# Kernel tuning notes

Measured on AMD Instinct MI355X. Metric: run time of the kernel, lower is better.

## Reference

```python
import jax, jax.numpy as jnp
import numpy as np

NEG_SLOPE = 0.01  # F.leaky_relu default
FGW = 0.1         # feature_guidance_weight


def gat_layer(x, src, dst, W, att_l, att_r, heads, out_ch, concat):
    N = x.shape[0]
    # reward-based guidance weights (L1-normalized over nodes, F.normalize p=1 dim=0)
    rw = 1.0 / (jnp.abs(x[:, -1:]) + 1e-6)                    # [N,1]
    rw = rw / jnp.maximum(jnp.sum(jnp.abs(rw), axis=0), 1e-12)
    h = (x @ W).reshape(N, heads, out_ch)                      # [N,H,C]
    # per-node attention halves, gathered per edge (avoids [E,H,C] for scores)
    al = jnp.sum(h * att_l, axis=-1)                           # [N,H] (x_i side)
    ar = jnp.sum(h * att_r, axis=-1)                           # [N,H] (x_j side)
    alpha = jax.nn.leaky_relu(al[dst] + ar[src], NEG_SLOPE)    # [E,H]
    alpha = alpha + FGW * jnp.log(rw[src])                     # guidance from source node
    # segment softmax over incoming edges of each target node (PyG softmax)
    m = jax.ops.segment_max(alpha, dst, num_segments=N)        # [N,H]
    e = jnp.exp(alpha - m[dst])
    s = jax.ops.segment_sum(e, dst, num_segments=N)
    alpha = e / (s[dst] + 1e-16)                               # [E,H]
    # weighted scatter-aggregate of source features
    msg = h[src] * alpha[:, :, None]                           # [E,H,C]
    out = jax.ops.segment_sum(msg, dst, num_segments=N)        # [N,H,C]
    if concat:
        return out.reshape(N, heads * out_ch)
    return out.mean(axis=1)


def setup_inputs() -> dict:
    key = jax.random.key(0)
    ks = jax.random.split(key, 10)
    N, E, D_IN, HID, HEADS, D_OUT = 50000, 800000, 128, 64, 4, 1

    def xavier(k, shape, fan_in, fan_out):
        a = jnp.sqrt(6.0 / (fan_in + fan_out))
        return jax.random.uniform(k, shape, jnp.float32, -a, a)

    x = jax.random.normal(ks[0], (N, D_IN), jnp.float32)
    edge_index = jax.random.randint(ks[1], (2, E), 0, N, jnp.int32)
    W1 = xavier(ks[2], (D_IN, HEADS * HID), D_IN, HEADS * HID)
    att_l1 = xavier(ks[3], (1, HEADS, HID), HID, HID)
    att_r1 = xavier(ks[4], (1, HEADS, HID), HID, HID)
    W2 = xavier(ks[5], (HEADS * HID, HID), HEADS * HID, HID)
    att_l2 = xavier(ks[6], (1, 1, HID), HID, HID)
    att_r2 = xavier(ks[7], (1, 1, HID), HID, HID)
    fc_w = xavier(ks[8], (HID, D_OUT), HID, D_OUT)
    fc_b = jnp.zeros((D_OUT,), jnp.float32)
    return {"x": x, "edge_index": edge_index, "W1": W1, "att_l1": att_l1,
            "att_r1": att_r1, "W2": W2, "att_l2": att_l2, "att_r2": att_r2,
            "fc_w": fc_w, "fc_b": fc_b}


def reference(x, edge_index, W1, att_l1, att_r1, W2, att_l2, att_r2, fc_w, fc_b):
    src, dst = edge_index[0], edge_index[1]
    HID, HEADS = 64, 4
    h = gat_layer(x, src, dst, W1, att_l1, att_r1, HEADS, HID, concat=True)
    h = jax.nn.elu(h)  # dropout omitted (eval mode)
    h = gat_layer(h, src, dst, W2, att_l2, att_r2, 1, HID, concat=False)
    h = jax.nn.elu(h)
    return h @ fc_w + fc_b
```

## Files before the change

kernel.cpp:

```cpp
#include <hip/hip_runtime.h>
#include <hip/hip_bf16.h>

typedef __hip_bfloat16 bf16;
typedef __attribute__((ext_vector_type(8))) short bf16x8;
typedef __attribute__((ext_vector_type(4))) float f32x4;

#define NEG_SLOPE 0.01f
#define FGW 0.1f

__device__ __forceinline__ float b2f(bf16 v) { return __bfloat162float(v); }

__device__ __forceinline__ float ldf(const void* p, size_t i, int isbf) {
    return isbf ? b2f(((const bf16*)p)[i]) : ((const float*)p)[i];
}

__device__ __forceinline__ float bu2f(unsigned short u) {
    return __uint_as_float(((unsigned)u) << 16);
}
__device__ __forceinline__ unsigned short f2bu(float f) {
    return __bfloat16_as_ushort(__float2bfloat16(f));
}

__device__ __forceinline__ float waveReduceSum(float v) {
#pragma unroll
    for (int o = 32; o > 0; o >>= 1) v += __shfl_down(v, o, 64);
    return v;
}

#define ATOMIC_ADD_F32(p, v) unsafeAtomicAdd((p), (v))

__global__ __launch_bounds__(256) void k_degdet(const int* __restrict__ ei, int* __restrict__ deg, int E,
                                                const unsigned short* __restrict__ xr,
                                                float* __restrict__ sscal, int* __restrict__ flag,
                                                const void* __restrict__ W1, const void* __restrict__ W2,
                                                unsigned short* __restrict__ Wp1h,
                                                unsigned short* __restrict__ Wp1l,
                                                unsigned short* __restrict__ Wp2) {
    __shared__ int sflag;
    const int t = threadIdx.x;
    const bool packer = (blockIdx.x < 128);
    if (packer) {
        if (t < 64) {
            int big = 0;
            for (int i = t; i < 256; i += 64) {
                int ex = (xr[i] >> 7) & 0xFF;
                if (ex >= 0xBF) big = 1;
            }
            unsigned long long mk = __ballot(big);
            if (t == 0) sflag = (mk == 0ull) ? 1 : 0;
        }
        __syncthreads();
        const int isbf = sflag;
        if (blockIdx.x == 0 && t == 0) {
            *flag = isbf;
            sscal[0] = 0.f; sscal[1] = 0.f;
        }
        int id = blockIdx.x * 256 + t;
        {
            int j = id & 7, l = (id >> 3) & 63, ko = (id >> 9) & 3, T = id >> 11;
            int k = ko * 32 + (l >> 4) * 8 + j, col = T * 16 + (l & 15);
            float wv = ldf(W1, (size_t)k * 256 + col, isbf);
            unsigned short hi = f2bu(wv);
            Wp1h[id] = hi;
            Wp1l[id] = f2bu(wv - bu2f(hi));
        }
        if (id < 16384) {
            int j = id & 7, l = (id >> 3) & 63, ko = (id >> 9) & 7, T = id >> 12;
            int k = ko * 32 + (l >> 4) * 8 + j, col = T * 16 + (l & 15);
            Wp2[id] = f2bu(ldf(W2, (size_t)k * 64 + col, isbf));
        }
    }
    int e = blockIdx.x * 256 + t;
    if (e < E) atomicAdd(&deg[ei[E + e]], 1);
}

__global__ __launch_bounds__(256) void k_scanA(const int* __restrict__ deg, int* __restrict__ tmp,
                                               int* __restrict__ bsum, int N) {
    __shared__ int part[256];
    const int t = threadIdx.x;
    int i = blockIdx.x * 256 + t;
    int v = (i < N) ? deg[i] : 0;
    part[t] = v;
    __syncthreads();
    for (int o = 1; o < 256; o <<= 1) {
        int add = (t >= o) ? part[t - o] : 0;
        __syncthreads();
        part[t] += add;
        __syncthreads();
    }
    if (i < N) tmp[i] = part[t];
    if (t == 255) bsum[blockIdx.x] = part[255];
}

__global__ __launch_bounds__(256) void k_scanB(int* __restrict__ bsum, int nb, int* __restrict__ rowptrN) {
    __shared__ int part[256];
    const int t = threadIdx.x;
    const int K = (nb + 255) / 256;
    int vs[8];
    int lsum = 0;
#pragma unroll
    for (int k = 0; k < 8; k++) {
        int idx = t * K + k;
        vs[k] = (k < K && idx < nb) ? bsum[idx] : 0;
        lsum += vs[k];
    }
    part[t] = lsum;
    __syncthreads();
    for (int o = 1; o < 256; o <<= 1) {
        int add = (t >= o) ? part[t - o] : 0;
        __syncthreads();
        part[t] += add;
        __syncthreads();
    }
    int excl = part[t] - lsum;
#pragma unroll
    for (int k = 0; k < 8; k++) {
        int idx = t * K + k;
        if (k < K && idx < nb) { bsum[idx] = excl; excl += vs[k]; }
    }
    if (t == 255) *rowptrN = part[255];
}

__global__ __launch_bounds__(256) void k_scanC(const int* __restrict__ deg, const int* __restrict__ tmp,
                                               const int* __restrict__ bsum, int* __restrict__ rowptr,
                                               int* __restrict__ cursor, int N) {
    int i = blockIdx.x * 256 + threadIdx.x;
    if (i >= N) return;
    rowptr[i] = bsum[blockIdx.x] + tmp[i] - deg[i];
    cursor[i] = 0;
}

__global__ __launch_bounds__(256) void k_scatter(const int* __restrict__ ei, const int* __restrict__ rowptr,
                                                 int* __restrict__ cursor, int* __restrict__ csr_src, int E) {
    int e = blockIdx.x * 256 + threadIdx.x;
    if (e >= E) return;
    int d = ei[E + e];
    int pos = atomicAdd(&cursor[d], 1);
    csr_src[rowptr[d] + pos] = ei[e];
}

__global__ __launch_bounds__(256) void k_gemm1f(const void* __restrict__ x,
                                                const unsigned short* __restrict__ Wp1h,
                                                const unsigned short* __restrict__ Wp1l,
                                                const void* __restrict__ attl,
                                                const void* __restrict__ attr,
                                                unsigned short* __restrict__ h1,
                                                float* __restrict__ pk1,
                                                float* __restrict__ al1,
                                                float* __restrict__ rwS,
                                                int N, const int* __restrict__ flag) {
    const int isbf = *flag;
    __shared__ unsigned short Ash[64 * 136];
    __shared__ unsigned short Asl[64 * 136];
    __shared__ float rpart[64];
    const int row0 = blockIdx.x * 64;
    const int t = threadIdx.x;
    const int w = t >> 6, lane = t & 63;
    const int m = lane & 15, quad = lane >> 4;

#pragma unroll
    for (int it = 0; it < 4; it++) {
        int idx = it * 256 + t;
        int r = idx >> 4, c = idx & 15;
        float v[8];
        if (row0 + r < N) {
            if (isbf) {
                const unsigned short* xu = (const unsigned short*)x;
                uint4 raw = *reinterpret_cast<const uint4*>(xu + (size_t)(row0 + r) * 128 + c * 8);
                const unsigned short* rs = (const unsigned short*)&raw;
#pragma unroll
                for (int k = 0; k < 8; k++) v[k] = bu2f(rs[k]);
            } else {
                const float* xf = (const float*)x;
                float4 a = *reinterpret_cast<const float4*>(xf + (size_t)(row0 + r) * 128 + c * 8);
                float4 b = *reinterpret_cast<const float4*>(xf + (size_t)(row0 + r) * 128 + c * 8 + 4);
                v[0] = a.x; v[1] = a.y; v[2] = a.z; v[3] = a.w;
                v[4] = b.x; v[5] = b.y; v[6] = b.z; v[7] = b.w;
            }
        } else {
#pragma unroll
            for (int k = 0; k < 8; k++) v[k] = 0.f;
        }
        unsigned short hi[8], lo[8];
#pragma unroll
        for (int k = 0; k < 8; k++) {
            hi[k] = f2bu(v[k]);
            lo[k] = f2bu(v[k] - bu2f(hi[k]));
        }
        *reinterpret_cast<uint4*>(&Ash[r * 136 + c * 8]) = *reinterpret_cast<const uint4*>(hi);
        *reinterpret_cast<uint4*>(&Asl[r * 136 + c * 8]) = *reinterpret_cast<const uint4*>(lo);
    }
    __syncthreads();

    bf16x8 Bh[4][4];
#pragma unroll
    for (int tt = 0; tt < 4; tt++)
#pragma unroll
        for (int ko = 0; ko < 4; ko++)
            Bh[tt][ko] = *reinterpret_cast<const bf16x8*>(
                &Wp1h[(size_t)(((w * 4 + tt) * 4 + ko) * 64 + lane) * 8]);
    float avl[4], avr[4];
#pragma unroll
    for (int tt = 0; tt < 4; tt++) {
        int col = (w * 4 + tt) * 16 + m;
        avl[tt] = ldf(attl, col, isbf);
        avr[tt] = ldf(attr, col, isbf);
    }
    for (int sub = 0; sub < 4; sub++) {
        const int rbase = sub * 16;
        bf16x8 Ah[4], Al[4];
#pragma unroll
        for (int ko = 0; ko < 4; ko++) {
            Ah[ko] = *reinterpret_cast<const bf16x8*>(&Ash[(rbase + m) * 136 + ko * 32 + quad * 8]);
            Al[ko] = *reinterpret_cast<const bf16x8*>(&Asl[(rbase + m) * 136 + ko * 32 + quad * 8]);
        }
        f32x4 Cf[4];
#pragma unroll
        for (int tt = 0; tt < 4; tt++) Cf[tt] = (f32x4){0.f, 0.f, 0.f, 0.f};
#pragma unroll
        for (int ko = 0; ko < 4; ko++)
#pragma unroll
            for (int tt = 0; tt < 4; tt++) {
                Cf[tt] = __builtin_amdgcn_mfma_f32_16x16x32_bf16(Ah[ko], Bh[tt][ko], Cf[tt], 0, 0, 0);
                Cf[tt] = __builtin_amdgcn_mfma_f32_16x16x32_bf16(Al[ko], Bh[tt][ko], Cf[tt], 0, 0, 0);
                bf16x8 Bl = *reinterpret_cast<const bf16x8*>(
                    &Wp1l[(size_t)(((w * 4 + tt) * 4 + ko) * 64 + lane) * 8]);
                Cf[tt] = __builtin_amdgcn_mfma_f32_16x16x32_bf16(Ah[ko], Bl, Cf[tt], 0, 0, 0);
            }
#pragma unroll
        for (int tt = 0; tt < 4; tt++) {
            int col = (w * 4 + tt) * 16 + m;
#pragma unroll
            for (int reg = 0; reg < 4; reg++) {
                int row = row0 + rbase + quad * 4 + reg;
                if (row < N) h1[(size_t)row * 256 + col] = f2bu(Cf[tt][reg]);
            }
        }
        if (w == 3 && m == 15) {
#pragma unroll
            for (int reg = 0; reg < 4; reg++) {
                int row = row0 + rbase + quad * 4 + reg;
                if (row < N) pk1[(size_t)row * 8 + 5] = Cf[3][reg];
            }
        }
        float sl[4], sr[4];
#pragma unroll
        for (int reg = 0; reg < 4; reg++) {
            float a = 0.f, b = 0.f;
#pragma unroll
            for (int tt = 0; tt < 4; tt++) {
                a = fmaf(avl[tt], Cf[tt][reg], a);
                b = fmaf(avr[tt], Cf[tt][reg], b);
            }
            sl[reg] = a; sr[reg] = b;
        }
#pragma unroll
        for (int off = 8; off >= 1; off >>= 1) {
#pragma unroll
            for (int reg = 0; reg < 4; reg++) {
                sl[reg] += __shfl_down(sl[reg], off, 64);
                sr[reg] += __shfl_down(sr[reg], off, 64);
            }
        }
        if (m == 0) {
#pragma unroll
            for (int reg = 0; reg < 4; reg++) {
                int row = row0 + rbase + quad * 4 + reg;
                if (row < N) {
                    al1[(size_t)row * 4 + w] = sl[reg];
                    pk1[(size_t)row * 8 + w] = sr[reg];
                }
            }
        }
    }
    if (t < 64) {
        int row = row0 + t;
        float rr = 0.f;
        if (row < N) {
            float a = fabsf(ldf(x, (size_t)row * 128 + 127, isbf));
            rr = 1.f / (a + 1e-6f);
            pk1[(size_t)row * 8 + 4] = logf(rr);
        }
        rpart[t] = rr;
    }
    __syncthreads();
    if (t == 0) {
        float s = 0.f;
#pragma unroll
        for (int i = 0; i < 64; i++) s += rpart[i];
        ATOMIC_ADD_F32(rwS, s);
    }
}

__global__ __launch_bounds__(256) void k_agg1(const int* __restrict__ rowptr,
                                              const int* __restrict__ csr_src,
                                              const float* __restrict__ al1,
                                              const float* __restrict__ pk1,
                                              const float* __restrict__ rwS,
                                              const unsigned short* __restrict__ h1,
                                              unsigned short* __restrict__ x2b,
                                              float* __restrict__ x2c, int N) {
    int d = blockIdx.x * 4 + (threadIdx.x >> 6);
    if (d >= N) return;
    const int lane = threadIdx.x & 63;
    const int q = lane & 15;
    const int g = lane >> 4;
    const int h = q >> 2;
    const bool last15 = (q == 15);
    const float gl = FGW * logf(fmaxf(*rwS, 1e-12f));
    const float al_h = al1[(size_t)d * 4 + h];
    const int beg = rowptr[d], end = rowptr[d + 1];

    const char* pk1c = (const char*)pk1;
    const char* h1c  = (const char*)h1;

    float acc[16];
#pragma unroll
    for (int k = 0; k < 16; k++) acc[k] = 0.f;
    float ssum = 0.f;

    for (int base = beg; base < end; base += 32) {
        const int lim = min(end - base, 32);
        const int nst = (lim + 3) >> 2;

        int sj[8];
#pragma unroll
        for (int k = 0; k < 8; k++)
            if (k < nst) sj[k] = csr_src[min(base + k * 4 + g, end - 1)];

        float arP[4]; float2 lcP[4]; uint4 h0P[4], h1P[4];

#define LD1(K) do {                                                                   \
        int s_ = sj[(K)];                                                             \
        unsigned po_ = (unsigned)s_ * 32u;                                            \
        arP[(K) & 3] = *reinterpret_cast<const float*>(pk1c + po_ + 4u * (unsigned)h);\
        lcP[(K) & 3] = *reinterpret_cast<const float2*>(pk1c + po_ + 16u);            \
        unsigned ho_ = (unsigned)s_ * 512u + (unsigned)q * 32u;                       \
        h0P[(K) & 3] = *reinterpret_cast<const uint4*>(h1c + ho_);                    \
        h1P[(K) & 3] = *reinterpret_cast<const uint4*>(h1c + ho_ + 16u);              \
    } while (0)

#define CONS1(K) do {                                                                 \
        bool cval_ = ((K) * 4 + g) < lim;                                             \
        float a_ = al_h + arP[(K) & 3];                                               \
        a_ = fmaxf(a_, NEG_SLOPE * a_);                                               \
        a_ = fmaf(FGW, lcP[(K) & 3].x, a_ - gl);                                      \
        float e_ = cval_ ? __expf(a_) : 0.f;                                          \
        ssum += e_;                                                                   \
        uint4 cb0_ = h0P[(K) & 3], cb1_ = h1P[(K) & 3];                               \
        unsigned uu_; float lo_, hi_;                                                 \
        uu_ = cb0_.x; lo_ = __uint_as_float(uu_ << 16); hi_ = __uint_as_float(uu_ & 0xFFFF0000u); \
        acc[0] = fmaf(e_, lo_, acc[0]);  acc[1] = fmaf(e_, hi_, acc[1]);              \
        uu_ = cb0_.y; lo_ = __uint_as_float(uu_ << 16); hi_ = __uint_as_float(uu_ & 0xFFFF0000u); \
        acc[2] = fmaf(e_, lo_, acc[2]);  acc[3] = fmaf(e_, hi_, acc[3]);              \
        uu_ = cb0_.z; lo_ = __uint_as_float(uu_ << 16); hi_ = __uint_as_float(uu_ & 0xFFFF0000u); \
        acc[4] = fmaf(e_, lo_, acc[4]);  acc[5] = fmaf(e_, hi_, acc[5]);              \
        uu_ = cb0_.w; lo_ = __uint_as_float(uu_ << 16); hi_ = __uint_as_float(uu_ & 0xFFFF0000u); \
        acc[6] = fmaf(e_, lo_, acc[6]);  acc[7] = fmaf(e_, hi_, acc[7]);              \
        uu_ = cb1_.x; lo_ = __uint_as_float(uu_ << 16); hi_ = __uint_as_float(uu_ & 0xFFFF0000u); \
        acc[8] = fmaf(e_, lo_, acc[8]);  acc[9] = fmaf(e_, hi_, acc[9]);              \
        uu_ = cb1_.y; lo_ = __uint_as_float(uu_ << 16); hi_ = __uint_as_float(uu_ & 0xFFFF0000u); \
        acc[10] = fmaf(e_, lo_, acc[10]); acc[11] = fmaf(e_, hi_, acc[11]);           \
        uu_ = cb1_.z; lo_ = __uint_as_float(uu_ << 16); hi_ = __uint_as_float(uu_ & 0xFFFF0000u); \
        acc[12] = fmaf(e_, lo_, acc[12]); acc[13] = fmaf(e_, hi_, acc[13]);           \
        uu_ = cb1_.w; lo_ = __uint_as_float(uu_ << 16); hi_ = __uint_as_float(uu_ & 0xFFFF0000u); \
        hi_ = last15 ? lcP[(K) & 3].y : hi_;    \
        acc[14] = fmaf(e_, lo_, acc[14]); acc[15] = fmaf(e_, hi_, acc[15]);           \
    } while (0)

        LD1(0);
        if (1 < nst) LD1(1);
        if (2 < nst) LD1(2);
#pragma unroll
        for (int k = 0; k < 8; k++) {
            if (k >= nst) break;
            if (k + 3 < 8 && k + 3 < nst) LD1(k + 3);
            CONS1(k);
        }
#undef LD1
#undef CONS1
    }

#pragma unroll
    for (int k = 0; k < 16; k++) {
        acc[k] += __shfl_xor(acc[k], 16, 64);
        acc[k] += __shfl_xor(acc[k], 32, 64);
    }
    ssum += __shfl_xor(ssum, 16, 64);
    ssum += __shfl_xor(ssum, 32, 64);

    const float inv = 1.f / (ssum + 1e-16f);
    float o0 = (g == 0 ? acc[0] : g == 1 ? acc[4]  : g == 2 ? acc[8]  : acc[12]);
    float o1 = (g == 0 ? acc[1] : g == 1 ? acc[5]  : g == 2 ? acc[9]  : acc[13]);
    float o2 = (g == 0 ? acc[2] : g == 1 ? acc[6]  : g == 2 ? acc[10] : acc[14]);
    float o3 = (g == 0 ? acc[3] : g == 1 ? acc[7]  : g == 2 ? acc[11] : acc[15]);
    o0 *= inv; o1 *= inv; o2 *= inv; o3 *= inv;
    o0 = (o0 > 0.f) ? o0 : expm1f(o0);
    o1 = (o1 > 0.f) ? o1 : expm1f(o1);
    o2 = (o2 > 0.f) ? o2 : expm1f(o2);
    o3 = (o3 > 0.f) ? o3 : expm1f(o3);
    uint2 ob;
    ob.x = (unsigned)f2bu(o0) | ((unsigned)f2bu(o1) << 16);
    ob.y = (unsigned)f2bu(o2) | ((unsigned)f2bu(o3) << 16);
    *reinterpret_cast<uint2*>(&x2b[(size_t)d * 256 + q * 16 + g * 4]) = ob;
    if (lane == 63) x2c[d] = o3;
}

__global__ __launch_bounds__(256) void k_gemm2f(const unsigned short* __restrict__ x2b,
                                                const float* __restrict__ x2c,
                                                const unsigned short* __restrict__ Wp2,
                                                const void* __restrict__ attl,
                                                const void* __restrict__ attr,
                                                unsigned short* __restrict__ h2,
                                                float* __restrict__ pk2,
                                                float* __restrict__ al2,
                                                float* __restrict__ rwS2,
                                                int N, const int* __restrict__ flag) {
    const int isbf = *flag;
    __shared__ unsigned short As[64 * 264];
    __shared__ float pl[4 * 64], pr[4 * 64], rpart[64];
    const int row0 = blockIdx.x * 64;
    const int t = threadIdx.x;
    const int w = t >> 6, lane = t & 63;
    const int m = lane & 15, quad = lane >> 4;
#pragma unroll
    for (int it = 0; it < 8; it++) {
        int idx = it * 256 + t;
        int r = idx >> 5, c = idx & 31;
        uint4 v = {0u, 0u, 0u, 0u};
        if (row0 + r < N)
            v = *reinterpret_cast<const uint4*>(x2b + (size_t)(row0 + r) * 256 + c * 8);
        *reinterpret_cast<uint4*>(&As[r * 264 + c * 8]) = v;
    }
    __syncthreads();
    bf16x8 Bf[8];
#pragma unroll
    for (int ko = 0; ko < 8; ko++)
        Bf[ko] = *reinterpret_cast<const bf16x8*>(&Wp2[(size_t)((w * 8 + ko) * 64 + lane) * 8]);
    f32x4 Cf[4];
#pragma unroll
    for (int sub = 0; sub < 4; sub++) Cf[sub] = (f32x4){0.f, 0.f, 0.f, 0.f};
#pragma unroll
    for (int ko = 0; ko < 8; ko++)
#pragma unroll
        for (int sub = 0; sub < 4; sub++) {
            bf16x8 Af = *reinterpret_cast<const bf16x8*>(
                &As[(sub * 16 + m) * 264 + ko * 32 + quad * 8]);
            Cf[sub] = __builtin_amdgcn_mfma_f32_16x16x32_bf16(Af, Bf[ko], Cf[sub], 0, 0, 0);
        }
    int col = w * 16 + m;
    float avl = ldf(attl, col, isbf);
    float avr = ldf(attr, col, isbf);
#pragma unroll
    for (int sub = 0; sub < 4; sub++) {
#pragma unroll
        for (int reg = 0; reg < 4; reg++) {
            int row = row0 + sub * 16 + quad * 4 + reg;
            if (row < N) h2[(size_t)row * 64 + col] = f2bu(Cf[sub][reg]);
        }
        float sl[4], sr[4];
#pragma unroll
        for (int reg = 0; reg < 4; reg++) { sl[reg] = avl * Cf[sub][reg]; sr[reg] = avr * Cf[sub][reg]; }
#pragma unroll
        for (int off = 8; off >= 1; off >>= 1) {
#pragma unroll
            for (int reg = 0; reg < 4; reg++) {
                sl[reg] += __shfl_down(sl[reg], off, 64);
                sr[reg] += __shfl_down(sr[reg], off, 64);
            }
        }
        if (m == 0) {
#pragma unroll
            for (int reg = 0; reg < 4; reg++) {
                pl[sub * 64 + w * 16 + quad * 4 + reg] = sl[reg];
                pr[sub * 64 + w * 16 + quad * 4 + reg] = sr[reg];
            }
        }
    }
    __syncthreads();
    if (t < 64) {
        int row = row0 + t;
        int sub = t >> 4, ri = t & 15;
        float rr = 0.f;
        if (row < N) {
            al2[row] = pl[sub * 64 + ri] + pl[sub * 64 + 16 + ri] + pl[sub * 64 + 32 + ri] + pl[sub * 64 + 48 + ri];
            pk2[(size_t)row * 2] = pr[sub * 64 + ri] + pr[sub * 64 + 16 + ri] + pr[sub * 64 + 32 + ri] + pr[sub * 64 + 48 + ri];
            float a = fabsf(x2c[row]);
            rr = 1.f / (a + 1e-6f);
            pk2[(size_t)row * 2 + 1] = logf(rr);
        }
        rpart[t] = rr;
    }
    __syncthreads();
    if (t == 0) {
        float s = 0.f;
#pragma unroll
        for (int i = 0; i < 64; i++) s += rpart[i];
        ATOMIC_ADD_F32(rwS2, s);
    }
}

__global__ __launch_bounds__(256) void k_agg2(const int* __restrict__ rowptr,
                                              const int* __restrict__ csr_src,
                                              const float* __restrict__ al2,
                                              const float* __restrict__ pk2,
                                              const float* __restrict__ rwS2,
                                              const unsigned short* __restrict__ h2,
                                              const void* __restrict__ fcw,
                                              const void* __restrict__ fcb,
                                              void* __restrict__ y, int N,
                                              const int* __restrict__ flag) {
    const int isbf = *flag;
    int d = blockIdx.x * 4 + (threadIdx.x >> 6);
    if (d >= N) return;
    const int lane = threadIdx.x & 63;
    const int q = lane & 15;
    const int g = lane >> 4;
    const float gl2 = FGW * logf(fmaxf(*rwS2, 1e-12f));
    const float al_d = al2[d];
    const int beg = rowptr[d], end = rowptr[d + 1];

    const char* pk2c = (const char*)pk2;
    const char* h2c  = (const char*)h2;

    float acc[4];
#pragma unroll
    for (int k = 0; k < 4; k++) acc[k] = 0.f;
    float ssum = 0.f;

    for (int base = beg; base < end; base += 32) {
        const int lim = min(end - base, 32);
        const int nst = (lim + 3) >> 2;

        int sj[8];
#pragma unroll
        for (int k = 0; k < 8; k++)
            if (k < nst) sj[k] = csr_src[min(base + k * 4 + g, end - 1)];

        float2 pvP[4]; uint2 hbP[4];

#define LD2(K) do {                                                                    \
        int s_ = sj[(K)];                                                              \
        pvP[(K) & 3] = *reinterpret_cast<const float2*>(pk2c + (unsigned)s_ * 8u);     \
        hbP[(K) & 3] = *reinterpret_cast<const uint2*>(h2c + (unsigned)s_ * 128u + (unsigned)q * 8u); \
    } while (0)

#define CONS2(K) do {                                                                  \
        bool cval_ = ((K) * 4 + g) < lim;                                              \
        float a_ = al_d + pvP[(K) & 3].x;                                              \
        a_ = fmaxf(a_, NEG_SLOPE * a_);                                                \
        a_ = fmaf(FGW, pvP[(K) & 3].y, a_ - gl2);                                      \
        float e_ = cval_ ? __expf(a_) : 0.f;                                           \
        ssum += e_;                                                                    \
        unsigned uu_ = hbP[(K) & 3].x;                                                 \
        acc[0] = fmaf(e_, __uint_as_float(uu_ << 16), acc[0]);                         \
        acc[1] = fmaf(e_, __uint_as_float(uu_ & 0xFFFF0000u), acc[1]);                 \
        uu_ = hbP[(K) & 3].y;                                                          \
        acc[2] = fmaf(e_, __uint_as_float(uu_ << 16), acc[2]);                         \
        acc[3] = fmaf(e_, __uint_as_float(uu_ & 0xFFFF0000u), acc[3]);                 \
    } while (0)

        LD2(0);
        if (1 < nst) LD2(1);
        if (2 < nst) LD2(2);
#pragma unroll
        for (int k = 0; k < 8; k++) {
            if (k >= nst) break;
            if (k + 3 < 8 && k + 3 < nst) LD2(k + 3);
            CONS2(k);
        }
#undef LD2
#undef CONS2
    }

#pragma unroll
    for (int k = 0; k < 4; k++) {
        acc[k] += __shfl_xor(acc[k], 16, 64);
        acc[k] += __shfl_xor(acc[k], 32, 64);
    }
    ssum += __shfl_xor(ssum, 16, 64);
    ssum += __shfl_xor(ssum, 32, 64);

    float v = (g == 0 ? acc[0] : g == 1 ? acc[1] : g == 2 ? acc[2] : acc[3]) / (ssum + 1e-16f);
    v = (v > 0.f) ? v : expm1f(v);
    float r = waveReduceSum(v * ldf(fcw, q * 4 + g, isbf));
    if (lane == 0) {
        float o = r + ldf(fcb, 0, isbf);
        if (isbf) ((bf16*)y)[d] = __float2bfloat16(o);
        else      ((float*)y)[d] = o;
    }
}

extern "C" void kernel_launch(void* const* d_in, const int* in_sizes, int n_in,
                              void* d_out, int out_size, void* d_ws, size_t ws_size,
                              hipStream_t stream) {
    const void* x     = d_in[0];
    const int*  ei    = (const int*)d_in[1];
    const void* W1    = d_in[2];
    const void* attl1 = d_in[3];
    const void* attr1 = d_in[4];
    const void* W2    = d_in[5];
    const void* attl2 = d_in[6];
    const void* attr2 = d_in[7];
    const void* fcw   = d_in[8];
    const void* fcb   = d_in[9];

    const int N = in_sizes[0] / 128;
    const int E = in_sizes[1] / 2;
    const int NB = (N + 255) / 256;

    float* p = (float*)d_ws;
    unsigned short* h1 = (unsigned short*)p; p += (size_t)N * 128;
    float* pk1    = p; p += (size_t)N * 8;
    float* al1    = p; p += (size_t)N * 4;
    unsigned short* x2b = (unsigned short*)p; p += (size_t)N * 128;
    float* x2c    = p; p += (size_t)N;
    float* pk2    = p; p += (size_t)N * 2;
    float* al2    = p; p += (size_t)N;
    int* rowptr   = (int*)p; p += (size_t)N + 1;
    int* deg      = (int*)p; p += (size_t)N;
    int* cursor   = (int*)p; p += (size_t)N;
    int* stmp     = (int*)p; p += (size_t)N;
    int* bsum     = (int*)p; p += (size_t)NB;
    int* csr_src  = (int*)p; p += (size_t)E;
    p = (float*)(((uintptr_t)p + 15) & ~(uintptr_t)15);
    unsigned short* Wp1h = (unsigned short*)p; p += 16384;
    unsigned short* Wp1l = (unsigned short*)p; p += 16384;
    unsigned short* Wp2  = (unsigned short*)p; p += 8192;
    float* sscal  = p; p += 4;
    int* dflag = (int*)(sscal + 2);

    unsigned short* h2 = h1;

    hipMemsetAsync(deg, 0, (size_t)N * 4, stream);

    k_degdet<<<(E + 255) / 256, 256, 0, stream>>>(ei, deg, E, (const unsigned short*)x, sscal, dflag,
                                                  W1, W2, Wp1h, Wp1l, Wp2);
    k_scanA<<<NB, 256, 0, stream>>>(deg, stmp, bsum, N);
    k_scanB<<<1, 256, 0, stream>>>(bsum, NB, &rowptr[N]);
    k_scanC<<<NB, 256, 0, stream>>>(deg, stmp, bsum, rowptr, cursor, N);
    k_scatter<<<(E + 255) / 256, 256, 0, stream>>>(ei, rowptr, cursor, csr_src, E);

    k_gemm1f<<<(N + 63) / 64, 256, 0, stream>>>(x, Wp1h, Wp1l, attl1, attr1, h1, pk1, al1,
                                                &sscal[0], N, dflag);
    k_agg1<<<(N + 3) / 4, 256, 0, stream>>>(rowptr, csr_src, al1, pk1,
                                            &sscal[0], h1, x2b, x2c, N);

    k_gemm2f<<<(N + 63) / 64, 256, 0, stream>>>(x2b, x2c, Wp2, attl2, attr2, h2, pk2, al2,
                                                &sscal[1], N, dflag);
    k_agg2<<<(N + 3) / 4, 256, 0, stream>>>(rowptr, csr_src, al2, pk2,
                                            &sscal[1], h2, fcw, fcb, d_out, N, dflag);
}
```

Before: 326.8 us.

## Pad CSR rows to multiples of four with dummy node, persistent aggregation grids

Each node's CSR row is padded to a multiple of four edges, and the padding points at a sentinel node N whose features are zero and whose score is -1e30. The aggregation kernels can then drop per-edge validity checks and clamped index loads. The aggregation kernels become grid-stride loops over at most 2048 blocks, and the first GEMM skips the split low-part MFMAs when the input is already bf16. This adds padding memory and extra sentinel writes, and the grid-stride loop may load-balance worse than one block per group of nodes.

```diff
diff --git a/kernel.cpp b/kernel.cpp
--- a/kernel.cpp
+++ b/kernel.cpp
@@ -79,7 +79,7 @@
     __shared__ int part[256];
     const int t = threadIdx.x;
     int i = blockIdx.x * 256 + t;
-    int v = (i < N) ? deg[i] : 0;
+    int v = (i < N) ? ((deg[i] + 3) & ~3) : 0;
     part[t] = v;
     __syncthreads();
     for (int o = 1; o < 256; o <<= 1) {
@@ -123,11 +123,15 @@
 
 __global__ __launch_bounds__(256) void k_scanC(const int* __restrict__ deg, const int* __restrict__ tmp,
                                                const int* __restrict__ bsum, int* __restrict__ rowptr,
-                                               int* __restrict__ cursor, int N) {
+                                               int* __restrict__ cursor, int* __restrict__ csr_src, int N) {
     int i = blockIdx.x * 256 + threadIdx.x;
     if (i >= N) return;
-    rowptr[i] = bsum[blockIdx.x] + tmp[i] - deg[i];
+    int dg = deg[i];
+    int pd = (dg + 3) & ~3;
+    int base = bsum[blockIdx.x] + tmp[i] - pd;
+    rowptr[i] = base;
     cursor[i] = 0;
+    for (int j = dg; j < pd; j++) csr_src[base + j] = N;
 }
 
 __global__ __launch_bounds__(256) void k_scatter(const int* __restrict__ ei, const int* __restrict__ rowptr,
@@ -158,6 +162,11 @@
     const int w = t >> 6, lane = t & 63;
     const int m = lane & 15, quad = lane >> 4;
 
+    if (blockIdx.x == 0) {
+        if (t < 32) *reinterpret_cast<uint4*>(&h1[(size_t)N * 256 + t * 8]) = (uint4){0u, 0u, 0u, 0u};
+        if (t < 8) pk1[(size_t)N * 8 + t] = (t < 4) ? -1e30f : 0.f;
+    }
+
 #pragma unroll
     for (int it = 0; it < 4; it++) {
         int idx = it * 256 + t;
@@ -181,14 +190,16 @@
 #pragma unroll
             for (int k = 0; k < 8; k++) v[k] = 0.f;
         }
-        unsigned short hi[8], lo[8];
-#pragma unroll
-        for (int k = 0; k < 8; k++) {
-            hi[k] = f2bu(v[k]);
-            lo[k] = f2bu(v[k] - bu2f(hi[k]));
-        }
+        unsigned short hi[8];
+#pragma unroll
+        for (int k = 0; k < 8; k++) hi[k] = f2bu(v[k]);
         *reinterpret_cast<uint4*>(&Ash[r * 136 + c * 8]) = *reinterpret_cast<const uint4*>(hi);
-        *reinterpret_cast<uint4*>(&Asl[r * 136 + c * 8]) = *reinterpret_cast<const uint4*>(lo);
+        if (!isbf) {
+            unsigned short lo[8];
+#pragma unroll
+            for (int k = 0; k < 8; k++) lo[k] = f2bu(v[k] - bu2f(hi[k]));
+            *reinterpret_cast<uint4*>(&Asl[r * 136 + c * 8]) = *reinterpret_cast<const uint4*>(lo);
+        }
     }
     __syncthreads();
 
@@ -208,25 +219,35 @@
     }
     for (int sub = 0; sub < 4; sub++) {
         const int rbase = sub * 16;
-        bf16x8 Ah[4], Al[4];
-#pragma unroll
-        for (int ko = 0; ko < 4; ko++) {
+        bf16x8 Ah[4];
+#pragma unroll
+        for (int ko = 0; ko < 4; ko++)
             Ah[ko] = *reinterpret_cast<const bf16x8*>(&Ash[(rbase + m) * 136 + ko * 32 + quad * 8]);
-            Al[ko] = *reinterpret_cast<const bf16x8*>(&Asl[(rbase + m) * 136 + ko * 32 + quad * 8]);
-        }
         f32x4 Cf[4];
 #pragma unroll
         for (int tt = 0; tt < 4; tt++) Cf[tt] = (f32x4){0.f, 0.f, 0.f, 0.f};
-#pragma unroll
-        for (int ko = 0; ko < 4; ko++)
-#pragma unroll
-            for (int tt = 0; tt < 4; tt++) {
-                Cf[tt] = __builtin_amdgcn_mfma_f32_16x16x32_bf16(Ah[ko], Bh[tt][ko], Cf[tt], 0, 0, 0);
-                Cf[tt] = __builtin_amdgcn_mfma_f32_16x16x32_bf16(Al[ko], Bh[tt][ko], Cf[tt], 0, 0, 0);
-                bf16x8 Bl = *reinterpret_cast<const bf16x8*>(
-                    &Wp1l[(size_t)(((w * 4 + tt) * 4 + ko) * 64 + lane) * 8]);
-                Cf[tt] = __builtin_amdgcn_mfma_f32_16x16x32_bf16(Ah[ko], Bl, Cf[tt], 0, 0, 0);
-            }
+        if (isbf) {
+#pragma unroll
+            for (int ko = 0; ko < 4; ko++)
+#pragma unroll
+                for (int tt = 0; tt < 4; tt++)
+                    Cf[tt] = __builtin_amdgcn_mfma_f32_16x16x32_bf16(Ah[ko], Bh[tt][ko], Cf[tt], 0, 0, 0);
+        } else {
+            bf16x8 Al[4];
+#pragma unroll
+            for (int ko = 0; ko < 4; ko++)
+                Al[ko] = *reinterpret_cast<const bf16x8*>(&Asl[(rbase + m) * 136 + ko * 32 + quad * 8]);
+#pragma unroll
+            for (int ko = 0; ko < 4; ko++)
+#pragma unroll
+                for (int tt = 0; tt < 4; tt++) {
+                    Cf[tt] = __builtin_amdgcn_mfma_f32_16x16x32_bf16(Ah[ko], Bh[tt][ko], Cf[tt], 0, 0, 0);
+                    Cf[tt] = __builtin_amdgcn_mfma_f32_16x16x32_bf16(Al[ko], Bh[tt][ko], Cf[tt], 0, 0, 0);
+                    bf16x8 Bl = *reinterpret_cast<const bf16x8*>(
+                        &Wp1l[(size_t)(((w * 4 + tt) * 4 + ko) * 64 + lane) * 8]);
+                    Cf[tt] = __builtin_amdgcn_mfma_f32_16x16x32_bf16(Ah[ko], Bl, Cf[tt], 0, 0, 0);
+                }
+        }
 #pragma unroll
         for (int tt = 0; tt < 4; tt++) {
             int col = (w * 4 + tt) * 16 + m;
@@ -300,52 +321,53 @@
                                               const unsigned short* __restrict__ h1,
                                               unsigned short* __restrict__ x2b,
                                               float* __restrict__ x2c, int N) {
-    int d = blockIdx.x * 4 + (threadIdx.x >> 6);
-    if (d >= N) return;
     const int lane = threadIdx.x & 63;
+    const int wid = threadIdx.x >> 6;
     const int q = lane & 15;
     const int g = lane >> 4;
     const int h = q >> 2;
     const bool last15 = (q == 15);
     const float gl = FGW * logf(fmaxf(*rwS, 1e-12f));
-    const float al_h = al1[(size_t)d * 4 + h];
-    const int beg = rowptr[d], end = rowptr[d + 1];
-
+    const unsigned qo = (unsigned)q * 32u;
+    const unsigned ho4 = (unsigned)h * 4u;
     const char* pk1c = (const char*)pk1;
     const char* h1c  = (const char*)h1;
-
-    float acc[16];
-#pragma unroll
-    for (int k = 0; k < 16; k++) acc[k] = 0.f;
-    float ssum = 0.f;
-
-    for (int base = beg; base < end; base += 32) {
-        const int lim = min(end - base, 32);
-        const int nst = (lim + 3) >> 2;
-
-        int sj[8];
-#pragma unroll
-        for (int k = 0; k < 8; k++)
-            if (k < nst) sj[k] = csr_src[min(base + k * 4 + g, end - 1)];
-
-        float arP[4]; float2 lcP[4]; uint4 h0P[4], h1P[4];
+    const int stride = gridDim.x * 4;
+
+    for (int d = blockIdx.x * 4 + wid; d < N; d += stride) {
+        const float al_h = al1[(size_t)d * 4 + h];
+        const int beg = rowptr[d], end = rowptr[d + 1];
+
+        float acc[16];
+#pragma unroll
+        for (int k = 0; k < 16; k++) acc[k] = 0.f;
+        float ssum = 0.f;
+
+        for (int base = beg; base < end; base += 32) {
+            const int nst = min(end - base, 32) >> 2;
+
+            int sj[8];
+#pragma unroll
+            for (int k = 0; k < 8; k++)
+                if (k < nst) sj[k] = csr_src[base + k * 4 + g];
+
+            float arP[4]; float2 lcP[4]; uint4 h0P[4], h1P[4];
 
 #define LD1(K) do {                                                                   \
         int s_ = sj[(K)];                                                             \
         unsigned po_ = (unsigned)s_ * 32u;                                            \
-        arP[(K) & 3] = *reinterpret_cast<const float*>(pk1c + po_ + 4u * (unsigned)h);\
+        arP[(K) & 3] = *reinterpret_cast<const float*>(pk1c + po_ + ho4);             \
         lcP[(K) & 3] = *reinterpret_cast<const float2*>(pk1c + po_ + 16u);            \
-        unsigned ho_ = (unsigned)s_ * 512u + (unsigned)q * 32u;                       \
+        unsigned ho_ = (unsigned)s_ * 512u + qo;                                      \
         h0P[(K) & 3] = *reinterpret_cast<const uint4*>(h1c + ho_);                    \
         h1P[(K) & 3] = *reinterpret_cast<const uint4*>(h1c + ho_ + 16u);              \
     } while (0)
 
 #define CONS1(K) do {                                                                 \
-        bool cval_ = ((K) * 4 + g) < lim;                                             \
         float a_ = al_h + arP[(K) & 3];                                               \
         a_ = fmaxf(a_, NEG_SLOPE * a_);                                               \
         a_ = fmaf(FGW, lcP[(K) & 3].x, a_ - gl);                                      \
-        float e_ = cval_ ? __expf(a_) : 0.f;                                          \
+        float e_ = __expf(a_);                                                        \
         ssum += e_;                                                                   \
         uint4 cb0_ = h0P[(K) & 3], cb1_ = h1P[(K) & 3];                               \
         unsigned uu_; float lo_, hi_;                                                 \
@@ -368,42 +390,43 @@
         acc[14] = fmaf(e_, lo_, acc[14]); acc[15] = fmaf(e_, hi_, acc[15]);           \
     } while (0)
 
-        LD1(0);
-        if (1 < nst) LD1(1);
-        if (2 < nst) LD1(2);
-#pragma unroll
-        for (int k = 0; k < 8; k++) {
-            if (k >= nst) break;
-            if (k + 3 < 8 && k + 3 < nst) LD1(k + 3);
-            CONS1(k);
-        }
+            LD1(0);
+            if (1 < nst) LD1(1);
+            if (2 < nst) LD1(2);
+#pragma unroll
+            for (int k = 0; k < 8; k++) {
+                if (k >= nst) break;
+                if (k + 3 < 8) { if (k + 3 < nst) LD1(k + 3); }
+                CONS1(k);
+            }
 #undef LD1
 #undef CONS1
-    }
-
-#pragma unroll
-    for (int k = 0; k < 16; k++) {
-        acc[k] += __shfl_xor(acc[k], 16, 64);
-        acc[k] += __shfl_xor(acc[k], 32, 64);
-    }
-    ssum += __shfl_xor(ssum, 16, 64);
-    ssum += __shfl_xor(ssum, 32, 64);
-
-    const float inv = 1.f / (ssum + 1e-16f);
-    float o0 = (g == 0 ? acc[0] : g == 1 ? acc[4]  : g == 2 ? acc[8]  : acc[12]);
-    float o1 = (g == 0 ? acc[1] : g == 1 ? acc[5]  : g == 2 ? acc[9]  : acc[13]);
-    float o2 = (g == 0 ? acc[2] : g == 1 ? acc[6]  : g == 2 ? acc[10] : acc[14]);
-    float o3 = (g == 0 ? acc[3] : g == 1 ? acc[7]  : g == 2 ? acc[11] : acc[15]);
-    o0 *= inv; o1 *= inv; o2 *= inv; o3 *= inv;
-    o0 = (o0 > 0.f) ? o0 : expm1f(o0);
-    o1 = (o1 > 0.f) ? o1 : expm1f(o1);
-    o2 = (o2 > 0.f) ? o2 : expm1f(o2);
-    o3 = (o3 > 0.f) ? o3 : expm1f(o3);
-    uint2 ob;
-    ob.x = (unsigned)f2bu(o0) | ((unsigned)f2bu(o1) << 16);
-    ob.y = (unsigned)f2bu(o2) | ((unsigned)f2bu(o3) << 16);
-    *reinterpret_cast<uint2*>(&x2b[(size_t)d * 256 + q * 16 + g * 4]) = ob;
-    if (lane == 63) x2c[d] = o3;
+        }
+
+#pragma unroll
+        for (int k = 0; k < 16; k++) {
+            acc[k] += __shfl_xor(acc[k], 16, 64);
+            acc[k] += __shfl_xor(acc[k], 32, 64);
+        }
+        ssum += __shfl_xor(ssum, 16, 64);
+        ssum += __shfl_xor(ssum, 32, 64);
+
+        const float inv = 1.f / (ssum + 1e-16f);
+        float o0 = (g == 0 ? acc[0] : g == 1 ? acc[4]  : g == 2 ? acc[8]  : acc[12]);
+        float o1 = (g == 0 ? acc[1] : g == 1 ? acc[5]  : g == 2 ? acc[9]  : acc[13]);
+        float o2 = (g == 0 ? acc[2] : g == 1 ? acc[6]  : g == 2 ? acc[10] : acc[14]);
+        float o3 = (g == 0 ? acc[3] : g == 1 ? acc[7]  : g == 2 ? acc[11] : acc[15]);
+        o0 *= inv; o1 *= inv; o2 *= inv; o3 *= inv;
+        o0 = (o0 > 0.f) ? o0 : expm1f(o0);
+        o1 = (o1 > 0.f) ? o1 : expm1f(o1);
+        o2 = (o2 > 0.f) ? o2 : expm1f(o2);
+        o3 = (o3 > 0.f) ? o3 : expm1f(o3);
+        uint2 ob;
+        ob.x = (unsigned)f2bu(o0) | ((unsigned)f2bu(o1) << 16);
+        ob.y = (unsigned)f2bu(o2) | ((unsigned)f2bu(o3) << 16);
+        *reinterpret_cast<uint2*>(&x2b[(size_t)d * 256 + q * 16 + g * 4]) = ob;
+        if (lane == 63) x2c[d] = o3;
+    }
 }
 
 __global__ __launch_bounds__(256) void k_gemm2f(const unsigned short* __restrict__ x2b,
@@ -423,6 +446,12 @@
     const int t = threadIdx.x;
     const int w = t >> 6, lane = t & 63;
     const int m = lane & 15, quad = lane >> 4;
+
+    if (blockIdx.x == 0) {
+        if (t < 8) *reinterpret_cast<uint4*>(&h2[(size_t)N * 64 + t * 8]) = (uint4){0u, 0u, 0u, 0u};
+        if (t == 0) { pk2[(size_t)N * 2] = -1e30f; pk2[(size_t)N * 2 + 1] = 0.f; }
+    }
+
 #pragma unroll
     for (int it = 0; it < 8; it++) {
         int idx = it * 256 + t;
@@ -511,46 +540,48 @@
                                               void* __restrict__ y, int N,
                                               const int* __restrict__ flag) {
     const int isbf = *flag;
-    int d = blockIdx.x * 4 + (threadIdx.x >> 6);
-    if (d >= N) return;
     const int lane = threadIdx.x & 63;
+    const int wid = threadIdx.x >> 6;
     const int q = lane & 15;
     const int g = lane >> 4;
     const float gl2 = FGW * logf(fmaxf(*rwS2, 1e-12f));
-    const float al_d = al2[d];
-    const int beg = rowptr[d], end = rowptr[d + 1];
-
     const char* pk2c = (const char*)pk2;
     const char* h2c  = (const char*)h2;
-
-    float acc[4];
-#pragma unroll
-    for (int k = 0; k < 4; k++) acc[k] = 0.f;
-    float ssum = 0.f;
-
-    for (int base = beg; base < end; base += 32) {
-        const int lim = min(end - base, 32);
-        const int nst = (lim + 3) >> 2;
-
-        int sj[8];
-#pragma unroll
-        for (int k = 0; k < 8; k++)
-            if (k < nst) sj[k] = csr_src[min(base + k * 4 + g, end - 1)];
-
-        float2 pvP[4]; uint2 hbP[4];
+    const unsigned qo8 = (unsigned)q * 8u;
+    const int stride = gridDim.x * 4;
+    const float fw = ldf(fcw, q * 4 + g, isbf);
+    const float fb = ldf(fcb, 0, isbf);
+
+    for (int d = blockIdx.x * 4 + wid; d < N; d += stride) {
+        const float al_d = al2[d];
+        const int beg = rowptr[d], end = rowptr[d + 1];
+
+        float acc[4];
+#pragma unroll
+        for (int k = 0; k < 4; k++) acc[k] = 0.f;
+        float ssum = 0.f;
+
+        for (int base = beg; base < end; base += 32) {
+            const int nst = min(end - base, 32) >> 2;
+
+            int sj[8];
+#pragma unroll
+            for (int k = 0; k < 8; k++)
+                if (k < nst) sj[k] = csr_src[base + k * 4 + g];
+
+            float2 pvP[4]; uint2 hbP[4];
 
 #define LD2(K) do {                                                                    \
         int s_ = sj[(K)];                                                              \
         pvP[(K) & 3] = *reinterpret_cast<const float2*>(pk2c + (unsigned)s_ * 8u);     \
-        hbP[(K) & 3] = *reinterpret_cast<const uint2*>(h2c + (unsigned)s_ * 128u + (unsigned)q * 8u); \
+        hbP[(K) & 3] = *reinterpret_cast<const uint2*>(h2c + (unsigned)s_ * 128u + qo8); \
     } while (0)
 
 #define CONS2(K) do {                                                                  \
-        bool cval_ = ((K) * 4 + g) < lim;                                              \
         float a_ = al_d + pvP[(K) & 3].x;                                              \
         a_ = fmaxf(a_, NEG_SLOPE * a_);                                                \
         a_ = fmaf(FGW, pvP[(K) & 3].y, a_ - gl2);                                      \
-        float e_ = cval_ ? __expf(a_) : 0.f;                                           \
+        float e_ = __expf(a_);                                                         \
         ssum += e_;                                                                    \
         unsigned uu_ = hbP[(K) & 3].x;                                                 \
         acc[0] = fmaf(e_, __uint_as_float(uu_ << 16), acc[0]);                         \
@@ -560,34 +591,35 @@
         acc[3] = fmaf(e_, __uint_as_float(uu_ & 0xFFFF0000u), acc[3]);                 \
     } while (0)
 
-        LD2(0);
-        if (1 < nst) LD2(1);
-        if (2 < nst) LD2(2);
-#pragma unroll
-        for (int k = 0; k < 8; k++) {
-            if (k >= nst) break;
-            if (k + 3 < 8 && k + 3 < nst) LD2(k + 3);
-            CONS2(k);
-        }
+            LD2(0);
+            if (1 < nst) LD2(1);
+            if (2 < nst) LD2(2);
+#pragma unroll
+            for (int k = 0; k < 8; k++) {
+                if (k >= nst) break;
+                if (k + 3 < 8) { if (k + 3 < nst) LD2(k + 3); }
+                CONS2(k);
+            }
 #undef LD2
 #undef CONS2
-    }
-
-#pragma unroll
-    for (int k = 0; k < 4; k++) {
-        acc[k] += __shfl_xor(acc[k], 16, 64);
-        acc[k] += __shfl_xor(acc[k], 32, 64);
-    }
-    ssum += __shfl_xor(ssum, 16, 64);
-    ssum += __shfl_xor(ssum, 32, 64);
-
-    float v = (g == 0 ? acc[0] : g == 1 ? acc[1] : g == 2 ? acc[2] : acc[3]) / (ssum + 1e-16f);
-    v = (v > 0.f) ? v : expm1f(v);
-    float r = waveReduceSum(v * ldf(fcw, q * 4 + g, isbf));
-    if (lane == 0) {
-        float o = r + ldf(fcb, 0, isbf);
-        if (isbf) ((bf16*)y)[d] = __float2bfloat16(o);
-        else      ((float*)y)[d] = o;
+        }
+
+#pragma unroll
+        for (int k = 0; k < 4; k++) {
+            acc[k] += __shfl_xor(acc[k], 16, 64);
+            acc[k] += __shfl_xor(acc[k], 32, 64);
+        }
+        ssum += __shfl_xor(ssum, 16, 64);
+        ssum += __shfl_xor(ssum, 32, 64);
+
+        float v = (g == 0 ? acc[0] : g == 1 ? acc[1] : g == 2 ? acc[2] : acc[3]) / (ssum + 1e-16f);
+        v = (v > 0.f) ? v : expm1f(v);
+        float r = waveReduceSum(v * fw);
+        if (lane == 0) {
+            float o = r + fb;
+            if (isbf) ((bf16*)y)[d] = __float2bfloat16(o);
+            else      ((float*)y)[d] = o;
+        }
     }
 }
 
@@ -608,21 +640,22 @@
     const int N = in_sizes[0] / 128;
     const int E = in_sizes[1] / 2;
     const int NB = (N + 255) / 256;
+    const int E2 = E + 4 * N;
 
     float* p = (float*)d_ws;
-    unsigned short* h1 = (unsigned short*)p; p += (size_t)N * 128;
-    float* pk1    = p; p += (size_t)N * 8;
+    unsigned short* h1 = (unsigned short*)p; p += (size_t)(N + 1) * 128;
+    float* pk1    = p; p += (size_t)(N + 1) * 8;
     float* al1    = p; p += (size_t)N * 4;
     unsigned short* x2b = (unsigned short*)p; p += (size_t)N * 128;
     float* x2c    = p; p += (size_t)N;
-    float* pk2    = p; p += (size_t)N * 2;
+    float* pk2    = p; p += (size_t)(N + 1) * 2;
     float* al2    = p; p += (size_t)N;
     int* rowptr   = (int*)p; p += (size_t)N + 1;
     int* deg      = (int*)p; p += (size_t)N;
     int* cursor   = (int*)p; p += (size_t)N;
     int* stmp     = (int*)p; p += (size_t)N;
     int* bsum     = (int*)p; p += (size_t)NB;
-    int* csr_src  = (int*)p; p += (size_t)E;
+    int* csr_src  = (int*)p; p += (size_t)E2;
     p = (float*)(((uintptr_t)p + 15) & ~(uintptr_t)15);
     unsigned short* Wp1h = (unsigned short*)p; p += 16384;
     unsigned short* Wp1l = (unsigned short*)p; p += 16384;
@@ -638,16 +671,18 @@
                                                   W1, W2, Wp1h, Wp1l, Wp2);
     k_scanA<<<NB, 256, 0, stream>>>(deg, stmp, bsum, N);
     k_scanB<<<1, 256, 0, stream>>>(bsum, NB, &rowptr[N]);
-    k_scanC<<<NB, 256, 0, stream>>>(deg, stmp, bsum, rowptr, cursor, N);
+    k_scanC<<<NB, 256, 0, stream>>>(deg, stmp, bsum, rowptr, cursor, csr_src, N);
     k_scatter<<<(E + 255) / 256, 256, 0, stream>>>(ei, rowptr, cursor, csr_src, E);
+
+    const int ag = min((N + 3) / 4, 2048);
 
     k_gemm1f<<<(N + 63) / 64, 256, 0, stream>>>(x, Wp1h, Wp1l, attl1, attr1, h1, pk1, al1,
                                                 &sscal[0], N, dflag);
-    k_agg1<<<(N + 3) / 4, 256, 0, stream>>>(rowptr, csr_src, al1, pk1,
-                                            &sscal[0], h1, x2b, x2c, N);
+    k_agg1<<<ag, 256, 0, stream>>>(rowptr, csr_src, al1, pk1,
+                                   &sscal[0], h1, x2b, x2c, N);
 
     k_gemm2f<<<(N + 63) / 64, 256, 0, stream>>>(x2b, x2c, Wp2, attl2, attr2, h2, pk2, al2,
                                                 &sscal[1], N, dflag);
-    k_agg2<<<(N + 3) / 4, 256, 0, stream>>>(rowptr, csr_src, al2, pk2,
-                                            &sscal[1], h2, fcw, fcb, d_out, N, dflag);
-}
+    k_agg2<<<ag, 256, 0, stream>>>(rowptr, csr_src, al2, pk2,
+                                   &sscal[1], h2, fcw, fcb, d_out, N, dflag);
+}
```

Measured after the change: 319.6 us. 1.02x faster.
